# Kernel tuning notes

Hardware: AMD Instinct MI355X
Metric: run time of the kernel (lower is better)

## Reference

```python
import jax, jax.numpy as jnp
import numpy as np

WD, WH, WW = 6, 6, 6
NUM_HEADS = 8
EPS = 1e-5


def setup_inputs() -> dict:
    key = jax.random.key(0)
    ks = jax.random.split(key, 4)
    B, C, D, H, W = 1, 128, 48, 48, 48
    return {
        "q_map": jax.random.normal(ks[0], (B, C, D, H, W), dtype=jnp.float32),
        "k_map": jax.random.normal(ks[1], (B, C, D, H, W), dtype=jnp.float32),
        "v_map": jax.random.normal(ks[2], (B, C, D, H, W), dtype=jnp.float32),
        "gamma_q": jnp.ones((C,), jnp.float32),
        "beta_q": jnp.zeros((C,), jnp.float32),
        "gamma_kv": jnp.ones((C,), jnp.float32),
        "beta_kv": jnp.zeros((C,), jnp.float32),
        "proj_w": jax.random.normal(ks[3], (C, C), dtype=jnp.float32) * (1.0 / np.sqrt(C)),
        "proj_b": jnp.zeros((C,), jnp.float32),
    }


def _layernorm(x, g, b):
    m = jnp.mean(x, axis=-1, keepdims=True)
    v = jnp.mean(jnp.square(x - m), axis=-1, keepdims=True)
    return (x - m) * jax.lax.rsqrt(v + EPS) * g + b


def _window_partition(x):
    # x: (B, D, H, W, C) -> windows: (B*nD*nH*nW, wd*wh*ww, C)
    B, D, H, W, C = x.shape
    pd, ph, pw = (WD - D % WD) % WD, (WH - H % WH) % WH, (WW - W % WW) % WW
    if pd or ph or pw:
        x = jnp.pad(x, ((0, 0), (0, pd), (0, ph), (0, pw), (0, 0)))
    Dp, Hp, Wp = D + pd, H + ph, W + pw
    x = x.reshape(B, Dp // WD, WD, Hp // WH, WH, Wp // WW, WW, C)
    x = jnp.transpose(x, (0, 1, 3, 5, 2, 4, 6, 7))
    return x.reshape(-1, WD * WH * WW, C), (D, H, W, Dp, Hp, Wp)


def _window_reverse(windows, meta):
    D, H, W, Dp, Hp, Wp = meta
    C = windows.shape[-1]
    nD, nH, nW = Dp // WD, Hp // WH, Wp // WW
    B = windows.shape[0] // (nD * nH * nW)
    x = windows.reshape(B, nD, nH, nW, WD, WH, WW, C)
    x = jnp.transpose(x, (0, 1, 4, 2, 5, 3, 6, 7)).reshape(B, Dp, Hp, Wp, C)
    return x[:, :D, :H, :W, :]


def reference(q_map, k_map, v_map, gamma_q, beta_q, gamma_kv, beta_kv, proj_w, proj_b):
    # (B, C, D, H, W) -> (B, D, H, W, C)
    q_map = jnp.transpose(q_map, (0, 2, 3, 4, 1))
    k_map = jnp.transpose(k_map, (0, 2, 3, 4, 1))
    v_map = jnp.transpose(v_map, (0, 2, 3, 4, 1))

    q, meta = _window_partition(q_map)
    k, _ = _window_partition(k_map)
    v, _ = _window_partition(v_map)

    q = _layernorm(q, gamma_q, beta_q)
    k = _layernorm(k, gamma_kv, beta_kv)
    v = _layernorm(v, gamma_kv, beta_kv)

    Bw, Nq, C = q.shape
    dh = C // NUM_HEADS
    q = q.reshape(Bw, Nq, NUM_HEADS, dh)
    k = k.reshape(Bw, -1, NUM_HEADS, dh)
    v = v.reshape(Bw, -1, NUM_HEADS, dh)

    scale = 1.0 / np.sqrt(dh).astype(np.float32)
    scores = jnp.einsum("bqhd,bkhd->bhqk", q, k) * scale  # (Bw, h, Nq, Nk)
    attn = jax.nn.softmax(scores, axis=-1)
    out = jnp.einsum("bhqk,bkhd->bqhd", attn, v).reshape(Bw, Nq, C)

    out = out @ proj_w.T + proj_b
    out = _window_reverse(out, meta)
    return jnp.transpose(out, (0, 4, 1, 2, 3))  # (B, C, D, H, W)
```

## Files before the change

kernel.cpp:

```cpp
#include <hip/hip_runtime.h>
#include <hip/hip_bf16.h>

typedef short s16x8 __attribute__((ext_vector_type(8)));
typedef float f32x2 __attribute__((ext_vector_type(2)));
typedef float f32x4 __attribute__((ext_vector_type(4)));
typedef float f32x16 __attribute__((ext_vector_type(16)));
typedef unsigned int u32;
typedef unsigned short u16;
typedef u32 u32x4v __attribute__((ext_vector_type(4)));

#define TOK 216
#define THREADS 448
#define SP 110592
#define BUF0 0
#define VOFF 57344
#define WOFF 122880
#define GBOFF 155648
#define LDS_OLD 157696
#define LDS_NEW 155648
#define TENB 28311552ull
#define WSNEED (3ull*TENB + 32768ull)

__device__ __forceinline__ u32 pack2(float a, float b) {
  u16 lo = __builtin_bit_cast(u16, __float2bfloat16(a));
  u16 hi = __builtin_bit_cast(u16, __float2bfloat16(b));
  return (u32)lo | ((u32)hi << 16);
}
__device__ __forceinline__ int swz(int row, int inner) {
  return inner ^ ((row & 7) << 4);
}
__device__ __forceinline__ void gload16(const void* g, void* l) {
  __builtin_amdgcn_global_load_lds(
      (const __attribute__((address_space(1))) void*)g,
      (__attribute__((address_space(3))) void*)l, 16, 0, 0);
}

__device__ __forceinline__ void ln_stats(const f32x2* xv, float& mA, float& rA,
                                         float& mB, float& rB) {
  float sA = 0.f, s2A = 0.f, sB = 0.f, s2B = 0.f;
#pragma unroll
  for (int c = 0; c < 32; ++c) {
    sA += xv[c].x; s2A += xv[c].x * xv[c].x;
    sB += xv[c].y; s2B += xv[c].y * xv[c].y;
  }
  sA += __shfl_xor(sA, 1); s2A += __shfl_xor(s2A, 1);
  sB += __shfl_xor(sB, 1); s2B += __shfl_xor(s2B, 1);
  sA += __shfl_xor(sA, 2); s2A += __shfl_xor(s2A, 2);
  sB += __shfl_xor(sB, 2); s2B += __shfl_xor(s2B, 2);
  mA = sA * (1.0f / 128.0f);
  rA = rsqrtf(s2A * (1.0f / 128.0f) - mA * mA + 1e-5f);
  mB = sB * (1.0f / 128.0f);
  rB = rsqrtf(s2B * (1.0f / 128.0f) - mB * mB + 1e-5f);
}

template<bool MASK>
__device__ __forceinline__ void attn_step(const char* smem, int h, int kt,
                                          s16x8 qfh, int lane,
                                          f32x16& acc, float& lsum) {
  const int half = lane >> 5;
  const int krow = kt * 32 + (lane & 31);
  s16x8 kf = *(const s16x8*)(smem + BUF0 + krow * 256 +
                             swz(krow, h * 32 + half * 16));
  __builtin_amdgcn_s_setprio(1);
  f32x16 st = __builtin_amdgcn_mfma_f32_32x32x16_bf16(kf, qfh, (f32x16){}, 0, 0, 0);
  __builtin_amdgcn_s_setprio(0);
  const int vrow = h * 16 + (lane & 15);
  s16x8 vf0 = *(const s16x8*)(smem + VOFF + vrow * 512 +
                              swz(vrow, kt * 64 + half * 16));
  s16x8 vf1 = *(const s16x8*)(smem + VOFF + vrow * 512 +
                              swz(vrow, kt * 64 + 32 + half * 16));
  const int NR = MASK ? 12 : 16;
  u32 A[8];
  float ts = 0.f;
#pragma unroll
  for (int i = 0; i < 8; ++i) {
    float p0 = (2 * i < NR) ? __expf(st[2 * i]) : 0.f;
    float p1 = (2 * i + 1 < NR) ? __expf(st[2 * i + 1]) : 0.f;
    ts += p0 + p1;
    A[i] = pack2(p0, p1);
  }
  lsum += ts;
  s16x8 pf0 = __builtin_bit_cast(s16x8, (u32x4v){A[0], A[1], A[2], A[3]});
  s16x8 pf1 = __builtin_bit_cast(s16x8, (u32x4v){A[4], A[5], A[6], A[7]});
  __builtin_amdgcn_s_setprio(1);
  acc = __builtin_amdgcn_mfma_f32_32x32x16_bf16(vf0, pf0, acc, 0, 0, 0);
  acc = __builtin_amdgcn_mfma_f32_32x32x16_bf16(vf1, pf1, acc, 0, 0, 0);
  __builtin_amdgcn_s_setprio(0);
}

extern "C" __global__ __launch_bounds__(256)
void lnpre_kernel(const float* __restrict__ qm, const float* __restrict__ km,
                  const float* __restrict__ vm,
                  const float* __restrict__ gq, const float* __restrict__ bq,
                  const float* __restrict__ gkv, const float* __restrict__ bkv,
                  const float* __restrict__ pw,
                  u16* __restrict__ qn, u16* __restrict__ kn,
                  u16* __restrict__ vn, u16* __restrict__ wbf) {
  const int tid = threadIdx.x;
  const int bid = blockIdx.x;
  if (bid >= 2304) {
#pragma unroll
    for (int k = 0; k < 32; ++k) {
      int idx = tid + 256 * k;
      f32x2 w2 = *(const f32x2*)(pw + idx * 2);
      ((u32*)wbf)[idx] = pack2(w2.x, w2.y);
    }
    return;
  }
  __shared__ float lf[6144];
  __shared__ float gb[512];
  const int d = bid / 48, h = bid - d * 48;
  const int dh = d * 2304 + h * 48;
  if (tid < 128) {
    gb[tid] = gq[tid]; gb[128 + tid] = bq[tid];
    gb[256 + tid] = gkv[tid]; gb[384 + tid] = bkv[tid];
  }
  const int w = tid >> 2, q = tid & 3;
#pragma unroll 1
  for (int t = 0; t < 3; ++t) {
    const float* src = t == 0 ? qm : (t == 1 ? km : vm);
    u16* dst = t == 0 ? qn : (t == 1 ? kn : vn);
    const float* g = (t == 0) ? gb : gb + 256;
    const float* b = (t == 0) ? gb + 128 : gb + 384;
    const float scale = (t == 0) ? 0.25f : 1.0f;
#pragma unroll
    for (int k = 0; k < 6; ++k) {
      int j = tid + 256 * k;
      int ch = j / 12, wq = j - ch * 12;
      *(f32x4*)(lf + ch * 48 + wq * 4) =
          *(const f32x4*)(src + (long)ch * SP + dh + wq * 4);
    }
    __syncthreads();
    if (tid < 192) {
      float s = 0.f, s2 = 0.f;
#pragma unroll
      for (int c = 0; c < 32; ++c) {
        float x = lf[(q + 4 * c) * 48 + w];
        s += x; s2 += x * x;
      }
      s += __shfl_xor(s, 1); s2 += __shfl_xor(s2, 1);
      s += __shfl_xor(s, 2); s2 += __shfl_xor(s2, 2);
      float m = s * (1.f / 128.f);
      float r = rsqrtf(s2 * (1.f / 128.f) - m * m + 1e-5f);
      u32* op = (u32*)(dst + (long)(dh + w) * 128 + 32 * q);
#pragma unroll
      for (int cc = 0; cc < 32; cc += 2) {
        int ch = 32 * q + cc;
        float y0 = ((lf[ch * 48 + w] - m) * r * g[ch] + b[ch]) * scale;
        float y1 = ((lf[(ch + 1) * 48 + w] - m) * r * g[ch + 1] + b[ch + 1]) * scale;
        op[cc >> 1] = pack2(y0, y1);
      }
    }
    __syncthreads();
  }
}

extern "C" __global__ __launch_bounds__(THREADS, 2)
void attn2_kernel(const u16* __restrict__ qn, const u16* __restrict__ kn,
                  const u16* __restrict__ vn, const u16* __restrict__ wbf,
                  const float* __restrict__ pb, float* __restrict__ out) {
  extern __shared__ __align__(16) char smem[];
  const int tid = threadIdx.x;
  const int lane = tid & 63;
  const int wv = tid >> 6;
  const int bid = blockIdx.x;
  const int wid = ((bid & 7) << 6) | (bid >> 3);
  const int wd = wid >> 6, wh = (wid >> 3) & 7, ww = wid & 7;
  const int wd6 = wd * 6, wh6 = wh * 6, ww6 = ww * 6;
  const int boff = wd6 * 2304 + wh6 * 48 + ww6;

  for (int uu = wv; uu < 140; uu += 7) {
    const u16* s; char* d;
    if (uu < 54) {
      int u = uu, row = 4 * u + (lane >> 4);
      int tq = row / 6;
      int g = (wd6 + tq / 6) * 2304 + (wh6 + tq % 6) * 48 + ww6 + row % 6;
      s = qn + g * 128 + (((lane & 15) ^ (row & 7)) << 3);
      d = smem + BUF0 + u * 1024;
    } else if (uu < 108) {
      int u = uu - 54, row = 4 * u + (lane >> 4);
      int tq = row / 6;
      int g = (wd6 + tq / 6) * 2304 + (wh6 + tq % 6) * 48 + ww6 + row % 6;
      s = vn + g * 128 + ((lane & 15) << 3);
      d = smem + VOFF + u * 1024;
    } else {
      int u = uu - 108, row = 4 * u + (lane >> 4);
      s = wbf + row * 128 + (((lane & 15) ^ (row & 7)) << 3);
      d = smem + WOFF + u * 1024;
    }
    gload16(s, d);
  }
  __syncthreads();

  s16x8 qf[8];
  {
    int row = wv * 32 + (lane & 31);
    int ib = (lane >> 5) * 16;
#pragma unroll
    for (int h = 0; h < 8; ++h)
      qf[h] = *(const s16x8*)(smem + BUF0 + row * 256 + swz(row, h * 32 + ib));
  }
  __syncthreads();

  for (int uu = wv; uu < 54; uu += 7) {
    int row = 4 * uu + (lane >> 4);
    int tq = row / 6;
    int g = (wd6 + tq / 6) * 2304 + (wh6 + tq % 6) * 48 + ww6 + row % 6;
    gload16(kn + g * 128 + (((lane & 15) ^ (row & 7)) << 3),
            smem + BUF0 + uu * 1024);
  }
  u32 tr[32];
#pragma unroll
  for (int k = 0; k < 16; ++k) {
    int u = tid + 448 * k;
    if (u < 6912) {
      int t = (u >> 6) * 2, c2 = u & 63;
      tr[2 * k]     = *(const u32*)(smem + VOFF + t * 256 + c2 * 4);
      tr[2 * k + 1] = *(const u32*)(smem + VOFF + t * 256 + 256 + c2 * 4);
    }
  }
  __syncthreads();

#pragma unroll
  for (int k = 0; k < 16; ++k) {
    int u = tid + 448 * k;
    if (u < 6912) {
      int t = (u >> 6) * 2, c2 = u & 63;
      int st = (t & ~12) | ((t & 4) << 1) | ((t & 8) >> 1);
      int c = 2 * c2;
      u32 w0 = (tr[2 * k] & 0xFFFFu) | (tr[2 * k + 1] << 16);
      u32 w1 = (tr[2 * k] >> 16) | (tr[2 * k + 1] & 0xFFFF0000u);
      *(u32*)(smem + VOFF + c * 512 + ((st * 2) ^ ((c & 7) << 4))) = w0;
      *(u32*)(smem + VOFF + (c + 1) * 512 + ((st * 2) ^ (((c + 1) & 7) << 4))) = w1;
    }
  }
  if (tid < 128) {
    int x = (tid & 7) << 4;
    *(u32*)(smem + VOFF + tid * 512 + (424 ^ x)) = 0;
    *(u32*)(smem + VOFF + tid * 512 + (428 ^ x)) = 0;
    *(u32*)(smem + VOFF + tid * 512 + (440 ^ x)) = 0;
    *(u32*)(smem + VOFF + tid * 512 + (444 ^ x)) = 0;
  }
  __syncthreads();

  u32 oPk[8][4];
#pragma unroll
  for (int hp = 0; hp < 4; ++hp) {
    const int h0 = hp * 2, h1 = h0 + 1;
    f32x16 a0 = {}, a1 = {};
    float l0 = 0.f, l1 = 0.f;
#pragma unroll 1
    for (int kt = 0; kt < 6; ++kt) {
      attn_step<false>(smem, h0, kt, qf[h0], lane, a0, l0);
      attn_step<false>(smem, h1, kt, qf[h1], lane, a1, l1);
    }
    attn_step<true>(smem, h0, 6, qf[h0], lane, a0, l0);
    attn_step<true>(smem, h1, 6, qf[h1], lane, a1, l1);
    l0 += __shfl_xor(l0, 32);
    l1 += __shfl_xor(l1, 32);
    float i0 = 1.0f / l0, i1 = 1.0f / l1;
#pragma unroll
    for (int r = 0; r < 4; ++r) {
      oPk[h0][r] = pack2(a0[2 * r] * i0, a0[2 * r + 1] * i0);
      oPk[h1][r] = pack2(a1[2 * r] * i1, a1[2 * r + 1] * i1);
    }
  }
  __syncthreads();

  {
    const int tok = wv * 32 + (lane & 31);
    const int half = lane >> 5;
#pragma unroll
    for (int h = 0; h < 8; ++h) {
      int chb = h * 32 + half * 8;
      *(u32*)(smem + BUF0 + tok * 256 + swz(tok, chb))      = oPk[h][0];
      *(u32*)(smem + BUF0 + tok * 256 + swz(tok, chb + 4))  = oPk[h][1];
      *(u32*)(smem + BUF0 + tok * 256 + swz(tok, chb + 16)) = oPk[h][2];
      *(u32*)(smem + BUF0 + tok * 256 + swz(tok, chb + 20)) = oPk[h][3];
    }
  }
  __syncthreads();

#pragma unroll 1
  for (int ti = 0; ti < 2; ++ti) {
    int tt = wv * 2 + ti;
    int tok = tt * 16 + (lane & 15);
    s16x8 bfr[4];
#pragma unroll
    for (int kk = 0; kk < 4; ++kk)
      bfr[kk] = *(const s16x8*)(smem + BUF0 + tok * 256 +
                                swz(tok, kk * 64 + (lane >> 4) * 16));
    bool tokValid = tok < TOK;
    int tdd = tok / 36, trr = tok - tdd * 36;
    int thh = trr / 6, tww = trr - thh * 6;
    int pos = boff + tdd * 2304 + thh * 48 + tww;
#pragma unroll 1
    for (int jt = 0; jt < 8; ++jt) {
      f32x4 acc = {};
#pragma unroll
      for (int kk = 0; kk < 4; ++kk) {
        int rw = jt * 16 + (lane & 15);
        s16x8 af = *(const s16x8*)(smem + WOFF + rw * 256 +
                                   swz(rw, kk * 64 + (lane >> 4) * 16));
        acc = __builtin_amdgcn_mfma_f32_16x16x32_bf16(af, bfr[kk], acc, 0, 0, 0);
      }
      f32x4 pbv = *(const f32x4*)(pb + jt * 16 + (lane >> 4) * 4);
      if (tokValid) {
#pragma unroll
        for (int r = 0; r < 4; ++r) {
          int j = jt * 16 + (lane >> 4) * 4 + r;
          out[j * SP + pos] = acc[r] + pbv[r];
        }
      }
    }
  }
}

extern "C" __global__ __launch_bounds__(THREADS, 2)
void ca3d_kernel(const float* __restrict__ qm, const float* __restrict__ km,
                 const float* __restrict__ vm,
                 const float* __restrict__ gq, const float* __restrict__ bq,
                 const float* __restrict__ gkv, const float* __restrict__ bkv,
                 const float* __restrict__ pw, const float* __restrict__ pb,
                 float* __restrict__ out) {
  extern __shared__ __align__(16) char smem[];
  const int tid = threadIdx.x;
  const int lane = tid & 63;
  const int wv = tid >> 6;
  const int bid = blockIdx.x;
  const int wid = ((bid & 7) << 6) | (bid >> 3);
  const int wd = wid >> 6, wh = (wid >> 3) & 7, ww = wid & 7;
  const int boff = wd * 6 * 2304 + wh * 6 * 48 + ww * 6;

  for (int i = tid * 16; i < VOFF + 65536; i += THREADS * 16)
    *(f32x4*)(smem + i) = (f32x4){};
  if (tid < 128) {
    ((float*)(smem + GBOFF))[tid] = gq[tid];
    ((float*)(smem + GBOFF + 512))[tid] = bq[tid];
    ((float*)(smem + GBOFF + 1024))[tid] = gkv[tid];
    ((float*)(smem + GBOFF + 1536))[tid] = bkv[tid];
  }
  const bool lnAct = tid < 432;
  const int tp = tid >> 2;
  const int cbase = (tid & 3) * 32;
  const int tA = tp * 2, tB = tA + 1;
  int td = tA / 36, tr_ = tA - td * 36;
  int th_ = tr_ / 6, tw_ = tr_ - th_ * 6;
  const int gpos = boff + td * 2304 + th_ * 48 + tw_;
  const int vposA = (tA & ~0xC) | ((tA & 4) << 1) | ((tA & 8) >> 1);

  f32x2 qv[32], kv[32], vv[32];
  if (lnAct) {
#pragma unroll
    for (int c = 0; c < 32; ++c)
      qv[c] = *(const f32x2*)(qm + gpos + (cbase + c) * SP);
#pragma unroll
    for (int c = 0; c < 32; ++c)
      kv[c] = *(const f32x2*)(km + gpos + (cbase + c) * SP);
  }
  __syncthreads();
  const float* gql = (const float*)(smem + GBOFF);
  const float* bql = (const float*)(smem + GBOFF + 512);
  const float* gkl = (const float*)(smem + GBOFF + 1024);
  const float* bkl = (const float*)(smem + GBOFF + 1536);
  if (lnAct) {
    float mA, rA, mB, rB;
    ln_stats(qv, mA, rA, mB, rB);
#pragma unroll
    for (int c = 0; c < 32; c += 2) {
      int cc = cbase + c;
      float g0 = gql[cc], g1 = gql[cc + 1], b0 = bql[cc], b1 = bql[cc + 1];
      *(u32*)(smem + BUF0 + tA * 256 + swz(tA, cc * 2)) =
          pack2(((qv[c].x - mA) * rA * g0 + b0) * 0.25f,
                ((qv[c + 1].x - mA) * rA * g1 + b1) * 0.25f);
      *(u32*)(smem + BUF0 + tB * 256 + swz(tB, cc * 2)) =
          pack2(((qv[c].y - mB) * rB * g0 + b0) * 0.25f,
                ((qv[c + 1].y - mB) * rB * g1 + b1) * 0.25f);
    }
#pragma unroll
    for (int c = 0; c < 32; ++c)
      vv[c] = *(const f32x2*)(vm + gpos + (cbase + c) * SP);
  }
  __syncthreads();
  s16x8 qf[8];
  {
    int row = wv * 32 + (lane & 31);
    int ib = (lane >> 5) * 16;
#pragma unroll
    for (int h = 0; h < 8; ++h)
      qf[h] = *(const s16x8*)(smem + BUF0 + row * 256 + swz(row, h * 32 + ib));
  }
  __syncthreads();
  if (lnAct) {
    {
      float mA, rA, mB, rB;
      ln_stats(kv, mA, rA, mB, rB);
#pragma unroll
      for (int c = 0; c < 32; c += 2) {
        int cc = cbase + c;
        float g0 = gkl[cc], g1 = gkl[cc + 1], b0 = bkl[cc], b1 = bkl[cc + 1];
        *(u32*)(smem + BUF0 + tA * 256 + swz(tA, cc * 2)) =
            pack2((kv[c].x - mA) * rA * g0 + b0,
                  (kv[c + 1].x - mA) * rA * g1 + b1);
        *(u32*)(smem + BUF0 + tB * 256 + swz(tB, cc * 2)) =
            pack2((kv[c].y - mB) * rB * g0 + b0,
                  (kv[c + 1].y - mB) * rB * g1 + b1);
      }
    }
    {
      float mA, rA, mB, rB;
      ln_stats(vv, mA, rA, mB, rB);
#pragma unroll
      for (int c = 0; c < 32; ++c) {
        int cc = cbase + c;
        float g0 = gkl[cc], b0 = bkl[cc];
        *(u32*)(smem + VOFF + cc * 512 + swz(cc, vposA * 2)) =
            pack2((vv[c].x - mA) * rA * g0 + b0,
                  (vv[c].y - mB) * rB * g0 + b0);
      }
    }
  }
  for (int i = tid; i < 8192; i += THREADS) {
    int j = i >> 6, c2 = i & 63;
    f32x2 w2 = *(const f32x2*)(pw + j * 128 + c2 * 2);
    *(u32*)(smem + WOFF + j * 256 + swz(j, c2 * 4)) = pack2(w2.x, w2.y);
  }
  __syncthreads();
  u32 oPk[8][4];
#pragma unroll
  for (int hp = 0; hp < 4; ++hp) {
    const int h0 = hp * 2, h1 = h0 + 1;
    f32x16 a0 = {}, a1 = {};
    float l0 = 0.f, l1 = 0.f;
#pragma unroll 1
    for (int kt = 0; kt < 6; ++kt) {
      attn_step<false>(smem, h0, kt, qf[h0], lane, a0, l0);
      attn_step<false>(smem, h1, kt, qf[h1], lane, a1, l1);
    }
    attn_step<true>(smem, h0, 6, qf[h0], lane, a0, l0);
    attn_step<true>(smem, h1, 6, qf[h1], lane, a1, l1);
    l0 += __shfl_xor(l0, 32);
    l1 += __shfl_xor(l1, 32);
    float i0 = 1.0f / l0, i1 = 1.0f / l1;
#pragma unroll
    for (int r = 0; r < 4; ++r) {
      oPk[h0][r] = pack2(a0[2 * r] * i0, a0[2 * r + 1] * i0);
      oPk[h1][r] = pack2(a1[2 * r] * i1, a1[2 * r + 1] * i1);
    }
  }
  __syncthreads();
  {
    const int tok = wv * 32 + (lane & 31);
    const int half = lane >> 5;
#pragma unroll
    for (int h = 0; h < 8; ++h) {
      int chb = h * 32 + half * 8;
      *(u32*)(smem + BUF0 + tok * 256 + swz(tok, chb))      = oPk[h][0];
      *(u32*)(smem + BUF0 + tok * 256 + swz(tok, chb + 4))  = oPk[h][1];
      *(u32*)(smem + BUF0 + tok * 256 + swz(tok, chb + 16)) = oPk[h][2];
      *(u32*)(smem + BUF0 + tok * 256 + swz(tok, chb + 20)) = oPk[h][3];
    }
  }
  __syncthreads();
#pragma unroll 1
  for (int ti = 0; ti < 2; ++ti) {
    int tt = wv * 2 + ti;
    int tok = tt * 16 + (lane & 15);
    s16x8 bfr[4];
#pragma unroll
    for (int kk = 0; kk < 4; ++kk)
      bfr[kk] = *(const s16x8*)(smem + BUF0 + tok * 256 +
                                swz(tok, kk * 64 + (lane >> 4) * 16));
    bool tokValid = tok < TOK;
    int tdd = tok / 36, trr = tok - tdd * 36;
    int thh = trr / 6, tww = trr - thh * 6;
    int pos = boff + tdd * 2304 + thh * 48 + tww;
#pragma unroll 1
    for (int jt = 0; jt < 8; ++jt) {
      f32x4 acc = {};
#pragma unroll
      for (int kk = 0; kk < 4; ++kk) {
        int rw = jt * 16 + (lane & 15);
        s16x8 af = *(const s16x8*)(smem + WOFF + rw * 256 +
                                   swz(rw, kk * 64 + (lane >> 4) * 16));
        acc = __builtin_amdgcn_mfma_f32_16x16x32_bf16(af, bfr[kk], acc, 0, 0, 0);
      }
      f32x4 pbv = *(const f32x4*)(pb + jt * 16 + (lane >> 4) * 4);
      if (tokValid) {
#pragma unroll
        for (int r = 0; r < 4; ++r) {
          int j = jt * 16 + (lane >> 4) * 4 + r;
          out[j * SP + pos] = acc[r] + pbv[r];
        }
      }
    }
  }
}

extern "C" void kernel_launch(void* const* d_in, const int* in_sizes, int n_in,
                              void* d_out, int out_size, void* d_ws, size_t ws_size,
                              hipStream_t stream) {
  const float* qm  = (const float*)d_in[0];
  const float* km  = (const float*)d_in[1];
  const float* vm  = (const float*)d_in[2];
  const float* gq  = (const float*)d_in[3];
  const float* bq  = (const float*)d_in[4];
  const float* gkv = (const float*)d_in[5];
  const float* bkv = (const float*)d_in[6];
  const float* pw  = (const float*)d_in[7];
  const float* pb  = (const float*)d_in[8];
  if (ws_size >= WSNEED) {
    u16* qn  = (u16*)d_ws;
    u16* kn  = (u16*)((char*)d_ws + TENB);
    u16* vn  = (u16*)((char*)d_ws + 2 * TENB);
    u16* wbf = (u16*)((char*)d_ws + 3 * TENB);
    hipLaunchKernelGGL(lnpre_kernel, dim3(2305), dim3(256), 0, stream,
                       qm, km, vm, gq, bq, gkv, bkv, pw, qn, kn, vn, wbf);
    hipLaunchKernelGGL(attn2_kernel, dim3(512), dim3(THREADS), LDS_NEW, stream,
                       qn, kn, vn, wbf, pb, (float*)d_out);
  } else {
    hipLaunchKernelGGL(ca3d_kernel, dim3(512), dim3(THREADS), LDS_OLD, stream,
                       qm, km, vm, gq, bq, gkv, bkv, pw, pb, (float*)d_out);
  }
}
```

Before: 155.7 us.

## Split heads across twice the waves in attention kernel, use exp2 softmax

The attention kernel now launches 896 threads (14 waves) per window instead of 448. Each query-row wave group handles 4 of the 8 heads rather than all 8, which halves per-wave registers and the serial MFMA chain, at the cost of 1 block per CU. The query scale now folds in log2(e) so softmax can use the hardware exp2 directly, and the sum is split into two accumulators. LayerNorm pre-pass stores are widened to 16-byte vector writes, and the K-loop is unrolled by 2.

```diff
diff --git a/kernel.cpp b/kernel.cpp
--- a/kernel.cpp
+++ b/kernel.cpp
@@ -10,7 +10,8 @@
 typedef u32 u32x4v __attribute__((ext_vector_type(4)));
 
 #define TOK 216
-#define THREADS 448
+#define T1 448
+#define T2 896
 #define SP 110592
 #define BUF0 0
 #define VOFF 57344
@@ -20,6 +21,7 @@
 #define LDS_NEW 155648
 #define TENB 28311552ull
 #define WSNEED (3ull*TENB + 32768ull)
+#define QSCALE 0.360673760f
 
 __device__ __forceinline__ u32 pack2(float a, float b) {
   u16 lo = __builtin_bit_cast(u16, __float2bfloat16(a));
@@ -71,15 +73,15 @@
                               swz(vrow, kt * 64 + 32 + half * 16));
   const int NR = MASK ? 12 : 16;
   u32 A[8];
-  float ts = 0.f;
+  float ts0 = 0.f, ts1 = 0.f;
 #pragma unroll
   for (int i = 0; i < 8; ++i) {
-    float p0 = (2 * i < NR) ? __expf(st[2 * i]) : 0.f;
-    float p1 = (2 * i + 1 < NR) ? __expf(st[2 * i + 1]) : 0.f;
-    ts += p0 + p1;
+    float p0 = (2 * i < NR) ? __builtin_amdgcn_exp2f(st[2 * i]) : 0.f;
+    float p1 = (2 * i + 1 < NR) ? __builtin_amdgcn_exp2f(st[2 * i + 1]) : 0.f;
+    if (i & 1) ts1 += p0 + p1; else ts0 += p0 + p1;
     A[i] = pack2(p0, p1);
   }
-  lsum += ts;
+  lsum += ts0 + ts1;
   s16x8 pf0 = __builtin_bit_cast(s16x8, (u32x4v){A[0], A[1], A[2], A[3]});
   s16x8 pf1 = __builtin_bit_cast(s16x8, (u32x4v){A[4], A[5], A[6], A[7]});
   __builtin_amdgcn_s_setprio(1);
@@ -122,7 +124,7 @@
     u16* dst = t == 0 ? qn : (t == 1 ? kn : vn);
     const float* g = (t == 0) ? gb : gb + 256;
     const float* b = (t == 0) ? gb + 128 : gb + 384;
-    const float scale = (t == 0) ? 0.25f : 1.0f;
+    const float scale = (t == 0) ? QSCALE : 1.0f;
 #pragma unroll
     for (int k = 0; k < 6; ++k) {
       int j = tid + 256 * k;
@@ -142,20 +144,25 @@
       s += __shfl_xor(s, 2); s2 += __shfl_xor(s2, 2);
       float m = s * (1.f / 128.f);
       float r = rsqrtf(s2 * (1.f / 128.f) - m * m + 1e-5f);
-      u32* op = (u32*)(dst + (long)(dh + w) * 128 + 32 * q);
-#pragma unroll
-      for (int cc = 0; cc < 32; cc += 2) {
-        int ch = 32 * q + cc;
-        float y0 = ((lf[ch * 48 + w] - m) * r * g[ch] + b[ch]) * scale;
-        float y1 = ((lf[(ch + 1) * 48 + w] - m) * r * g[ch + 1] + b[ch + 1]) * scale;
-        op[cc >> 1] = pack2(y0, y1);
+      u32x4v* op = (u32x4v*)(dst + (long)(dh + w) * 128 + 32 * q);
+#pragma unroll
+      for (int v4 = 0; v4 < 4; ++v4) {
+        u32x4v pk;
+#pragma unroll
+        for (int e = 0; e < 4; ++e) {
+          int ch = 32 * q + v4 * 8 + 2 * e;
+          float y0 = ((lf[ch * 48 + w] - m) * r * g[ch] + b[ch]) * scale;
+          float y1 = ((lf[(ch + 1) * 48 + w] - m) * r * g[ch + 1] + b[ch + 1]) * scale;
+          pk[e] = pack2(y0, y1);
+        }
+        op[v4] = pk;
       }
     }
     __syncthreads();
   }
 }
 
-extern "C" __global__ __launch_bounds__(THREADS, 2)
+extern "C" __global__ __launch_bounds__(T2, 1)
 void attn2_kernel(const u16* __restrict__ qn, const u16* __restrict__ kn,
                   const u16* __restrict__ vn, const u16* __restrict__ wbf,
                   const float* __restrict__ pb, float* __restrict__ out) {
@@ -163,13 +170,15 @@
   const int tid = threadIdx.x;
   const int lane = tid & 63;
   const int wv = tid >> 6;
+  const int wq = wv % 7;
+  const int hb = (wv / 7) * 4;
   const int bid = blockIdx.x;
   const int wid = ((bid & 7) << 6) | (bid >> 3);
   const int wd = wid >> 6, wh = (wid >> 3) & 7, ww = wid & 7;
   const int wd6 = wd * 6, wh6 = wh * 6, ww6 = ww * 6;
   const int boff = wd6 * 2304 + wh6 * 48 + ww6;
 
-  for (int uu = wv; uu < 140; uu += 7) {
+  for (int uu = wv; uu < 140; uu += 14) {
     const u16* s; char* d;
     if (uu < 54) {
       int u = uu, row = 4 * u + (lane >> 4);
@@ -192,27 +201,28 @@
   }
   __syncthreads();
 
-  s16x8 qf[8];
+  s16x8 qf[4];
   {
-    int row = wv * 32 + (lane & 31);
+    int row = wq * 32 + (lane & 31);
     int ib = (lane >> 5) * 16;
 #pragma unroll
-    for (int h = 0; h < 8; ++h)
-      qf[h] = *(const s16x8*)(smem + BUF0 + row * 256 + swz(row, h * 32 + ib));
-  }
-  __syncthreads();
-
-  for (int uu = wv; uu < 54; uu += 7) {
+    for (int j = 0; j < 4; ++j)
+      qf[j] = *(const s16x8*)(smem + BUF0 + row * 256 +
+                              swz(row, (hb + j) * 32 + ib));
+  }
+  __syncthreads();
+
+  for (int uu = wv; uu < 54; uu += 14) {
     int row = 4 * uu + (lane >> 4);
     int tq = row / 6;
     int g = (wd6 + tq / 6) * 2304 + (wh6 + tq % 6) * 48 + ww6 + row % 6;
     gload16(kn + g * 128 + (((lane & 15) ^ (row & 7)) << 3),
             smem + BUF0 + uu * 1024);
   }
-  u32 tr[32];
-#pragma unroll
-  for (int k = 0; k < 16; ++k) {
-    int u = tid + 448 * k;
+  u32 tr[16];
+#pragma unroll
+  for (int k = 0; k < 8; ++k) {
+    int u = tid + 896 * k;
     if (u < 6912) {
       int t = (u >> 6) * 2, c2 = u & 63;
       tr[2 * k]     = *(const u32*)(smem + VOFF + t * 256 + c2 * 4);
@@ -222,8 +232,8 @@
   __syncthreads();
 
 #pragma unroll
-  for (int k = 0; k < 16; ++k) {
-    int u = tid + 448 * k;
+  for (int k = 0; k < 8; ++k) {
+    int u = tid + 896 * k;
     if (u < 6912) {
       int t = (u >> 6) * 2, c2 = u & 63;
       int st = (t & ~12) | ((t & 4) << 1) | ((t & 8) >> 1);
@@ -243,48 +253,46 @@
   }
   __syncthreads();
 
-  u32 oPk[8][4];
-#pragma unroll
-  for (int hp = 0; hp < 4; ++hp) {
-    const int h0 = hp * 2, h1 = h0 + 1;
+  u32 oPk[4][4];
+#pragma unroll
+  for (int hp = 0; hp < 2; ++hp) {
+    const int h0 = hb + 2 * hp, h1 = h0 + 1;
     f32x16 a0 = {}, a1 = {};
     float l0 = 0.f, l1 = 0.f;
-#pragma unroll 1
+#pragma unroll 2
     for (int kt = 0; kt < 6; ++kt) {
-      attn_step<false>(smem, h0, kt, qf[h0], lane, a0, l0);
-      attn_step<false>(smem, h1, kt, qf[h1], lane, a1, l1);
-    }
-    attn_step<true>(smem, h0, 6, qf[h0], lane, a0, l0);
-    attn_step<true>(smem, h1, 6, qf[h1], lane, a1, l1);
+      attn_step<false>(smem, h0, kt, qf[2 * hp], lane, a0, l0);
+      attn_step<false>(smem, h1, kt, qf[2 * hp + 1], lane, a1, l1);
+    }
+    attn_step<true>(smem, h0, 6, qf[2 * hp], lane, a0, l0);
+    attn_step<true>(smem, h1, 6, qf[2 * hp + 1], lane, a1, l1);
     l0 += __shfl_xor(l0, 32);
     l1 += __shfl_xor(l1, 32);
     float i0 = 1.0f / l0, i1 = 1.0f / l1;
 #pragma unroll
     for (int r = 0; r < 4; ++r) {
-      oPk[h0][r] = pack2(a0[2 * r] * i0, a0[2 * r + 1] * i0);
-      oPk[h1][r] = pack2(a1[2 * r] * i1, a1[2 * r + 1] * i1);
+      oPk[2 * hp][r]     = pack2(a0[2 * r] * i0, a0[2 * r + 1] * i0);
+      oPk[2 * hp + 1][r] = pack2(a1[2 * r] * i1, a1[2 * r + 1] * i1);
     }
   }
   __syncthreads();
 
   {
-    const int tok = wv * 32 + (lane & 31);
+    const int tok = wq * 32 + (lane & 31);
     const int half = lane >> 5;
 #pragma unroll
-    for (int h = 0; h < 8; ++h) {
-      int chb = h * 32 + half * 8;
-      *(u32*)(smem + BUF0 + tok * 256 + swz(tok, chb))      = oPk[h][0];
-      *(u32*)(smem + BUF0 + tok * 256 + swz(tok, chb + 4))  = oPk[h][1];
-      *(u32*)(smem + BUF0 + tok * 256 + swz(tok, chb + 16)) = oPk[h][2];
-      *(u32*)(smem + BUF0 + tok * 256 + swz(tok, chb + 20)) = oPk[h][3];
-    }
-  }
-  __syncthreads();
-
-#pragma unroll 1
-  for (int ti = 0; ti < 2; ++ti) {
-    int tt = wv * 2 + ti;
-    int tok = tt * 16 + (lane & 15);
+    for (int j = 0; j < 4; ++j) {
+      int chb = (hb + j) * 32 + half * 8;
+      *(u32*)(smem + BUF0 + tok * 256 + swz(tok, chb))      = oPk[j][0];
+      *(u32*)(smem + BUF0 + tok * 256 + swz(tok, chb + 4))  = oPk[j][1];
+      *(u32*)(smem + BUF0 + tok * 256 + swz(tok, chb + 16)) = oPk[j][2];
+      *(u32*)(smem + BUF0 + tok * 256 + swz(tok, chb + 20)) = oPk[j][3];
+    }
+  }
+  __syncthreads();
+
+  {
+    int tok = wv * 16 + (lane & 15);
     s16x8 bfr[4];
 #pragma unroll
     for (int kk = 0; kk < 4; ++kk)
@@ -316,7 +324,7 @@
   }
 }
 
-extern "C" __global__ __launch_bounds__(THREADS, 2)
+extern "C" __global__ __launch_bounds__(T1, 2)
 void ca3d_kernel(const float* __restrict__ qm, const float* __restrict__ km,
                  const float* __restrict__ vm,
                  const float* __restrict__ gq, const float* __restrict__ bq,
@@ -332,7 +340,7 @@
   const int wd = wid >> 6, wh = (wid >> 3) & 7, ww = wid & 7;
   const int boff = wd * 6 * 2304 + wh * 6 * 48 + ww * 6;
 
-  for (int i = tid * 16; i < VOFF + 65536; i += THREADS * 16)
+  for (int i = tid * 16; i < VOFF + 65536; i += T1 * 16)
     *(f32x4*)(smem + i) = (f32x4){};
   if (tid < 128) {
     ((float*)(smem + GBOFF))[tid] = gq[tid];
@@ -371,11 +379,11 @@
       int cc = cbase + c;
       float g0 = gql[cc], g1 = gql[cc + 1], b0 = bql[cc], b1 = bql[cc + 1];
       *(u32*)(smem + BUF0 + tA * 256 + swz(tA, cc * 2)) =
-          pack2(((qv[c].x - mA) * rA * g0 + b0) * 0.25f,
-                ((qv[c + 1].x - mA) * rA * g1 + b1) * 0.25f);
+          pack2(((qv[c].x - mA) * rA * g0 + b0) * QSCALE,
+                ((qv[c + 1].x - mA) * rA * g1 + b1) * QSCALE);
       *(u32*)(smem + BUF0 + tB * 256 + swz(tB, cc * 2)) =
-          pack2(((qv[c].y - mB) * rB * g0 + b0) * 0.25f,
-                ((qv[c + 1].y - mB) * rB * g1 + b1) * 0.25f);
+          pack2(((qv[c].y - mB) * rB * g0 + b0) * QSCALE,
+                ((qv[c + 1].y - mB) * rB * g1 + b1) * QSCALE);
     }
 #pragma unroll
     for (int c = 0; c < 32; ++c)
@@ -420,7 +428,7 @@
       }
     }
   }
-  for (int i = tid; i < 8192; i += THREADS) {
+  for (int i = tid; i < 8192; i += T1) {
     int j = i >> 6, c2 = i & 63;
     f32x2 w2 = *(const f32x2*)(pw + j * 128 + c2 * 2);
     *(u32*)(smem + WOFF + j * 256 + swz(j, c2 * 4)) = pack2(w2.x, w2.y);
@@ -516,10 +524,10 @@
     u16* wbf = (u16*)((char*)d_ws + 3 * TENB);
     hipLaunchKernelGGL(lnpre_kernel, dim3(2305), dim3(256), 0, stream,
                        qm, km, vm, gq, bq, gkv, bkv, pw, qn, kn, vn, wbf);
-    hipLaunchKernelGGL(attn2_kernel, dim3(512), dim3(THREADS), LDS_NEW, stream,
+    hipLaunchKernelGGL(attn2_kernel, dim3(512), dim3(T2), LDS_NEW, stream,
                        qn, kn, vn, wbf, pb, (float*)d_out);
   } else {
-    hipLaunchKernelGGL(ca3d_kernel, dim3(512), dim3(THREADS), LDS_OLD, stream,
+    hipLaunchKernelGGL(ca3d_kernel, dim3(512), dim3(T1), LDS_OLD, stream,
                        qm, km, vm, gq, bq, gkv, bkv, pw, pb, (float*)d_out);
   }
 }
```

Result: no change. 154.2 us (-0.9%).
